# Optimization experiments

Hardware: AMD Instinct MI355X
Metric: run time of the kernel (lower is better)

## Reference

```python
import jax, jax.numpy as jnp
from jax import lax
import numpy as np

IN, HID, OUT = 28, 64, 10


def _lstm_layer(x_seq, W_ih, W_hh, b_ih, b_hh):
    # x_seq: [B, T, in]; PyTorch gate order: i, f, g, o (stacked along 4H)
    B = x_seq.shape[0]
    H = W_hh.shape[1]
    # Precompute input projection for all timesteps: [B, T, 4H]
    x_proj = jnp.einsum('bti,gi->btg', x_seq, W_ih) + b_ih + b_hh

    def step(carry, xt):
        h, c = carry
        gates = xt + h @ W_hh.T  # [B, 4H]
        i, f, g, o = jnp.split(gates, 4, axis=-1)
        i = jax.nn.sigmoid(i)
        f = jax.nn.sigmoid(f)
        g = jnp.tanh(g)
        o = jax.nn.sigmoid(o)
        c = f * c + i * g
        h = o * jnp.tanh(c)
        return (h, c), h

    h0 = jnp.zeros((B, H), x_seq.dtype)
    (_, _), hs = lax.scan(step, (h0, h0), jnp.swapaxes(x_proj, 0, 1))
    return jnp.swapaxes(hs, 0, 1)  # [B, T, H]


def setup_inputs() -> dict:
    key = jax.random.key(0)
    ks = jax.random.split(key, 12)
    s_in = 1.0 / np.sqrt(HID)
    u = lambda k, shape: jax.random.uniform(k, shape, jnp.float32, -s_in, s_in)
    return {
        'x': jax.random.normal(ks[0], (16384, 1, 28, 28), jnp.float32),
        'W_ih0': u(ks[1], (4 * HID, IN)),
        'W_hh0': u(ks[2], (4 * HID, HID)),
        'b_ih0': u(ks[3], (4 * HID,)),
        'b_hh0': u(ks[4], (4 * HID,)),
        'W_ih1': u(ks[5], (4 * HID, HID)),
        'W_hh1': u(ks[6], (4 * HID, HID)),
        'b_ih1': u(ks[7], (4 * HID,)),
        'b_hh1': u(ks[8], (4 * HID,)),
        'W_lin': u(ks[9], (OUT, HID)),
        'b_lin': u(ks[10], (OUT,)),
    }


def reference(x, W_ih0, W_hh0, b_ih0, b_hh0, W_ih1, W_hh1, b_ih1, b_hh1, W_lin, b_lin):
    # (N, C, H, W) -> (N, C*H, W): sequence of rows, feature = W = 28
    x = x.reshape(x.shape[0], -1, x.shape[-1])
    h1 = _lstm_layer(x, W_ih0, W_hh0, b_ih0, b_hh0)   # [B, T, 64]
    h2 = _lstm_layer(h1, W_ih1, W_hh1, b_ih1, b_hh1)  # [B, T, 64]
    last = h2[:, -1, :]
    return last @ W_lin.T + b_lin  # [B, 10]
```

## Files before the change

kernel.cpp:

```cpp
#include <hip/hip_runtime.h>


typedef _Float16 half8 __attribute__((ext_vector_type(8)));
typedef float floatx4 __attribute__((ext_vector_type(4)));

__device__ __forceinline__ float sigf(float v) {
    return __builtin_amdgcn_rcpf(1.0f + __expf(-v));
}
__device__ __forceinline__ float tanhf2(float v) {
    return 1.0f - 2.0f * __builtin_amdgcn_rcpf(__expf(2.0f * v) + 1.0f);
}

__launch_bounds__(512, 4)
__global__ void lstm_mfma(const float* __restrict__ x,
                          const float* __restrict__ Wih0, const float* __restrict__ Whh0,
                          const float* __restrict__ bih0, const float* __restrict__ bhh0,
                          const float* __restrict__ Wih1, const float* __restrict__ Whh1,
                          const float* __restrict__ bih1, const float* __restrict__ bhh1,
                          const float* __restrict__ Wlin, const float* __restrict__ blin,
                          float* __restrict__ out) {
    __shared__ __align__(16) _Float16 h0p[2][2048];
    __shared__ __align__(16) _Float16 h1p[2][2048];
    __shared__ __align__(16) _Float16 xb[2][1024];
    __shared__ float wlin_s[640];
    __shared__ float blin_s[10];

    const int lane = threadIdx.x;
    const int w    = threadIdx.y;
    const int tid  = w * 64 + lane;
    const int quad = lane >> 4;
    const int col  = lane & 15;

    half8 A0[2][3], A1[2][4];
    #pragma unroll
    for (int im = 0; im < 2; ++im) {
        int mt = 2 * w + im;
        int m  = mt * 16 + col;
        int u  = m >> 2, g = m & 3;
        int row = g * 64 + u;
        #pragma unroll
        for (int kt = 0; kt < 3; ++kt) {
            half8 r;
            #pragma unroll
            for (int j = 0; j < 8; ++j) {
                int k = kt * 32 + quad * 8 + j;
                float v;
                if (k < 28)       v = Wih0[row * 28 + k];
                else if (k == 28) v = bih0[row] + bhh0[row];
                else if (k < 32)  v = 0.f;
                else              v = Whh0[row * 64 + (k - 32)];
                r[j] = (_Float16)v;
            }
            A0[im][kt] = r;
        }
        #pragma unroll
        for (int kt = 0; kt < 4; ++kt) {
            half8 r;
            #pragma unroll
            for (int j = 0; j < 8; ++j) {
                int k = kt * 32 + quad * 8 + j;
                float v = (k < 64) ? Wih1[row * 64 + k] : Whh1[row * 64 + (k - 64)];
                r[j] = (_Float16)v;
            }
            A1[im][kt] = r;
        }
    }
    floatx4 bias1[2];
    #pragma unroll
    for (int im = 0; im < 2; ++im) {
        int u = (2 * w + im) * 4 + quad;
        #pragma unroll
        for (int r = 0; r < 4; ++r) bias1[im][r] = bih1[r * 64 + u] + bhh1[r * 64 + u];
    }

    int xrd[2], hrd[2][2], hwr[2][2];
    #pragma unroll
    for (int in = 0; in < 2; ++in) {
        xrd[in] = in * 512 + lane * 8;
        #pragma unroll
        for (int kt = 0; kt < 2; ++kt) hrd[kt][in] = (in * 2 + kt) * 512 + lane * 8;
        #pragma unroll
        for (int im = 0; im < 2; ++im) {
            int u = (2 * w + im) * 4 + quad;
            hwr[im][in] = (in * 2 + (u >> 5)) * 512 + (((u >> 3) & 3) * 16 + col) * 8 + (u & 7);
        }
    }

    const int xi = tid & 31;
    const bool xvalid = xi < 28;
    const float* xg[2];
    int xstg[2];
    #pragma unroll
    for (int s = 0; s < 2; ++s) {
        int b = (tid >> 5) + s * 16;
        xg[s]   = x + (blockIdx.x * 32 + b) * 784 + xi;
        xstg[s] = (b >> 4) * 512 + ((xi >> 3) * 16 + (b & 15)) * 8 + (xi & 7);
    }

    {
        int* z0 = (int*)&h0p[1][0];
        int* z1 = (int*)&h1p[1][0];
        #pragma unroll
        for (int i = tid; i < 1024; i += 512) { z0[i] = 0; z1[i] = 0; }
        #pragma unroll
        for (int s = 0; s < 2; ++s) {
            float xv = xvalid ? xg[s][0] : 0.f;
            xb[0][xstg[s]] = (xi == 28) ? (_Float16)1.0f : (_Float16)xv;
        }
    }
    __syncthreads();

    float c0[4] = {0.f, 0.f, 0.f, 0.f};
    float c1[4] = {0.f, 0.f, 0.f, 0.f};

    for (int p = -1; p <= 27; ++p) {
        const int pr  = p & 1;
        const int pr1 = pr ^ 1;
        const bool doL0 = (p < 27);
        const bool doL1 = (p >= 0);

        float xn[2] = {0.f, 0.f};
        if (p <= 25) {
            #pragma unroll
            for (int s = 0; s < 2; ++s)
                if (xvalid) xn[s] = xg[s][(p + 2) * 28];
        }

        half8 bh0[2][2];
        #pragma unroll
        for (int kt = 0; kt < 2; ++kt)
            #pragma unroll
            for (int in = 0; in < 2; ++in)
                bh0[kt][in] = *(const half8*)&h0p[pr][hrd[kt][in]];

        if (doL0) {
            floatx4 acc0[2][2];
            #pragma unroll
            for (int im = 0; im < 2; ++im)
                #pragma unroll
                for (int in = 0; in < 2; ++in)
                    acc0[im][in] = (floatx4){0.f, 0.f, 0.f, 0.f};
            #pragma unroll
            for (int in = 0; in < 2; ++in) {
                half8 bf = *(const half8*)&xb[pr1][xrd[in]];
                #pragma unroll
                for (int im = 0; im < 2; ++im)
                    acc0[im][in] = __builtin_amdgcn_mfma_f32_16x16x32_f16(A0[im][0], bf, acc0[im][in], 0, 0, 0);
            }
            #pragma unroll
            for (int kt = 0; kt < 2; ++kt)
                #pragma unroll
                for (int in = 0; in < 2; ++in)
                    #pragma unroll
                    for (int im = 0; im < 2; ++im)
                        acc0[im][in] = __builtin_amdgcn_mfma_f32_16x16x32_f16(A0[im][kt + 1], bh0[kt][in], acc0[im][in], 0, 0, 0);
            #pragma unroll
            for (int im = 0; im < 2; ++im) {
                #pragma unroll
                for (int in = 0; in < 2; ++in) {
                    floatx4 a = acc0[im][in];
                    float ig = sigf(a[0]), fg = sigf(a[1]), gg = tanhf2(a[2]), og = sigf(a[3]);
                    float c = fg * c0[im * 2 + in] + ig * gg;
                    c0[im * 2 + in] = c;
                    h0p[pr1][hwr[im][in]] = (_Float16)(og * tanhf2(c));
                }
            }
        }

        if (doL1) {
            floatx4 acc1[2][2];
            #pragma unroll
            for (int im = 0; im < 2; ++im)
                #pragma unroll
                for (int in = 0; in < 2; ++in)
                    acc1[im][in] = bias1[im];
            #pragma unroll
            for (int kt = 0; kt < 2; ++kt)
                #pragma unroll
                for (int in = 0; in < 2; ++in)
                    #pragma unroll
                    for (int im = 0; im < 2; ++im)
                        acc1[im][in] = __builtin_amdgcn_mfma_f32_16x16x32_f16(A1[im][kt], bh0[kt][in], acc1[im][in], 0, 0, 0);
            #pragma unroll
            for (int kt = 0; kt < 2; ++kt) {
                #pragma unroll
                for (int in = 0; in < 2; ++in) {
                    half8 bf = *(const half8*)&h1p[pr1][hrd[kt][in]];
                    #pragma unroll
                    for (int im = 0; im < 2; ++im)
                        acc1[im][in] = __builtin_amdgcn_mfma_f32_16x16x32_f16(A1[im][kt + 2], bf, acc1[im][in], 0, 0, 0);
                }
            }
            #pragma unroll
            for (int im = 0; im < 2; ++im) {
                #pragma unroll
                for (int in = 0; in < 2; ++in) {
                    floatx4 a = acc1[im][in];
                    float ig = sigf(a[0]), fg = sigf(a[1]), gg = tanhf2(a[2]), og = sigf(a[3]);
                    float c = fg * c1[im * 2 + in] + ig * gg;
                    c1[im * 2 + in] = c;
                    h1p[pr][hwr[im][in]] = (_Float16)(og * tanhf2(c));
                }
            }
        }

        if (p <= 25) {
            #pragma unroll
            for (int s = 0; s < 2; ++s)
                xb[pr][xstg[s]] = (xi == 28) ? (_Float16)1.0f : (_Float16)xn[s];
        }
        __syncthreads();
    }

    #pragma unroll
    for (int i = tid; i < 640; i += 512) wlin_s[i] = Wlin[i];
    if (tid < 10) blin_s[tid] = blin[tid];
    __syncthreads();
    if (tid < 320) {
        int b = tid / 10, o = tid - b * 10;
        float a = blin_s[o];
        #pragma unroll 8
        for (int u = 0; u < 64; ++u) {
            float hv = (float)h1p[1][((b >> 4) * 2 + (u >> 5)) * 512 + (((u >> 3) & 3) * 16 + (b & 15)) * 8 + (u & 7)];
            a += wlin_s[o * 64 + u] * hv;
        }
        out[(blockIdx.x * 32 + b) * 10 + o] = a;
    }
}

extern "C" void kernel_launch(void* const* d_in, const int* in_sizes, int n_in,
                              void* d_out, int out_size, void* d_ws, size_t ws_size,
                              hipStream_t stream) {
    const float* x    = (const float*)d_in[0];
    const float* Wih0 = (const float*)d_in[1];
    const float* Whh0 = (const float*)d_in[2];
    const float* bih0 = (const float*)d_in[3];
    const float* bhh0 = (const float*)d_in[4];
    const float* Wih1 = (const float*)d_in[5];
    const float* Whh1 = (const float*)d_in[6];
    const float* bih1 = (const float*)d_in[7];
    const float* bhh1 = (const float*)d_in[8];
    const float* Wlin = (const float*)d_in[9];
    const float* blin = (const float*)d_in[10];
    float* out = (float*)d_out;

    lstm_mfma<<<512, dim3(64, 8), 0, stream>>>(x, Wih0, Whh0, bih0, bhh0,
                                               Wih1, Whh1, bih1, bhh1, Wlin, blin, out);
}
```

Measured before the change: 197.9 us.

## Peel wavefront prologue/epilogue, interleave layer MFMAs, batch gate transcendentals

The skewed two-layer time loop is split into a peeled prologue (layer 0 only), a steady-state loop with no per-iteration branches, and a peeled epilogue (layer 1 only). In the steady state all LDS operands are loaded up front and the layer-0 and layer-1 MFMAs are interleaved so independent accumulator chains can overlap. Gate math is batched so all exps and reciprocals for the four tiles are issued together, raising instruction-level parallelism. Launch bounds drop from 4 to 2 blocks per CU, which allows more registers per thread but may lower occupancy.

```diff
diff --git a/kernel.cpp b/kernel.cpp
--- a/kernel.cpp
+++ b/kernel.cpp
@@ -4,14 +4,42 @@
 typedef _Float16 half8 __attribute__((ext_vector_type(8)));
 typedef float floatx4 __attribute__((ext_vector_type(4)));
 
-__device__ __forceinline__ float sigf(float v) {
-    return __builtin_amdgcn_rcpf(1.0f + __expf(-v));
+__device__ __forceinline__ void gate_batch4(const floatx4 (&acc)[2][2], float (&c)[4],
+                                            _Float16* __restrict__ plane,
+                                            const int (&hwr)[2][2]) {
+    float ei[4], ef[4], eg[4], eo[4];
+    #pragma unroll
+    for (int tt = 0; tt < 4; ++tt) {
+        floatx4 a = acc[tt >> 1][tt & 1];
+        ei[tt] = __expf(-a[0]);
+        ef[tt] = __expf(-a[1]);
+        eg[tt] = __expf(2.0f * a[2]);
+        eo[tt] = __expf(-a[3]);
+    }
+    float ri[4], rf[4], rg[4], ro[4];
+    #pragma unroll
+    for (int tt = 0; tt < 4; ++tt) {
+        ri[tt] = __builtin_amdgcn_rcpf(1.0f + ei[tt]);
+        rf[tt] = __builtin_amdgcn_rcpf(1.0f + ef[tt]);
+        rg[tt] = __builtin_amdgcn_rcpf(1.0f + eg[tt]);
+        ro[tt] = __builtin_amdgcn_rcpf(1.0f + eo[tt]);
+    }
+    float ec[4];
+    #pragma unroll
+    for (int tt = 0; tt < 4; ++tt) {
+        float tg = 1.0f - 2.0f * rg[tt];
+        float cn = rf[tt] * c[tt] + ri[tt] * tg;
+        c[tt] = cn;
+        ec[tt] = __expf(2.0f * cn);
+    }
+    #pragma unroll
+    for (int tt = 0; tt < 4; ++tt) {
+        float tc = 1.0f - 2.0f * __builtin_amdgcn_rcpf(ec[tt] + 1.0f);
+        plane[hwr[tt >> 1][tt & 1]] = (_Float16)(ro[tt] * tc);
+    }
 }
-__device__ __forceinline__ float tanhf2(float v) {
-    return 1.0f - 2.0f * __builtin_amdgcn_rcpf(__expf(2.0f * v) + 1.0f);
-}
-
-__launch_bounds__(512, 4)
+
+__launch_bounds__(512, 2)
 __global__ void lstm_mfma(const float* __restrict__ x,
                           const float* __restrict__ Wih0, const float* __restrict__ Whh0,
                           const float* __restrict__ bih0, const float* __restrict__ bhh0,
@@ -113,102 +141,122 @@
     float c0[4] = {0.f, 0.f, 0.f, 0.f};
     float c1[4] = {0.f, 0.f, 0.f, 0.f};
 
-    for (int p = -1; p <= 27; ++p) {
+    {
+        float xn[2] = {0.f, 0.f};
+        #pragma unroll
+        for (int s = 0; s < 2; ++s)
+            if (xvalid) xn[s] = xg[s][28];
+
+        floatx4 acc0[2][2];
+        #pragma unroll
+        for (int im = 0; im < 2; ++im)
+            #pragma unroll
+            for (int in = 0; in < 2; ++in)
+                acc0[im][in] = (floatx4){0.f, 0.f, 0.f, 0.f};
+        #pragma unroll
+        for (int in = 0; in < 2; ++in) {
+            half8 bf = *(const half8*)&xb[0][xrd[in]];
+            #pragma unroll
+            for (int im = 0; im < 2; ++im)
+                acc0[im][in] = __builtin_amdgcn_mfma_f32_16x16x32_f16(A0[im][0], bf, acc0[im][in], 0, 0, 0);
+        }
+        #pragma unroll
+        for (int kt = 0; kt < 2; ++kt) {
+            #pragma unroll
+            for (int in = 0; in < 2; ++in) {
+                half8 bf = *(const half8*)&h0p[1][hrd[kt][in]];
+                #pragma unroll
+                for (int im = 0; im < 2; ++im)
+                    acc0[im][in] = __builtin_amdgcn_mfma_f32_16x16x32_f16(A0[im][kt + 1], bf, acc0[im][in], 0, 0, 0);
+            }
+        }
+        gate_batch4(acc0, c0, &h0p[0][0], hwr);
+        #pragma unroll
+        for (int s = 0; s < 2; ++s)
+            xb[1][xstg[s]] = (xi == 28) ? (_Float16)1.0f : (_Float16)xn[s];
+        __syncthreads();
+    }
+
+    for (int p = 0; p < 27; ++p) {
         const int pr  = p & 1;
         const int pr1 = pr ^ 1;
-        const bool doL0 = (p < 27);
-        const bool doL1 = (p >= 0);
-
+        const _Float16* h0r = &h0p[pr][0];
+        _Float16*       h0w = &h0p[pr1][0];
+        const _Float16* h1r = &h1p[pr1][0];
+        _Float16*       h1w = &h1p[pr][0];
+        const _Float16* xr  = &xb[pr1][0];
+        _Float16*       xw  = &xb[pr][0];
+
+        const int xoff = (p < 26 ? p + 2 : 27) * 28;
         float xn[2] = {0.f, 0.f};
-        if (p <= 25) {
-            #pragma unroll
-            for (int s = 0; s < 2; ++s)
-                if (xvalid) xn[s] = xg[s][(p + 2) * 28];
-        }
-
-        half8 bh0[2][2];
+        #pragma unroll
+        for (int s = 0; s < 2; ++s)
+            if (xvalid) xn[s] = xg[s][xoff];
+
+        half8 bh0[2][2], bh1[2][2], bx[2];
+        #pragma unroll
+        for (int in = 0; in < 2; ++in) {
+            bx[in] = *(const half8*)&xr[xrd[in]];
+            #pragma unroll
+            for (int kt = 0; kt < 2; ++kt) {
+                bh0[kt][in] = *(const half8*)&h0r[hrd[kt][in]];
+                bh1[kt][in] = *(const half8*)&h1r[hrd[kt][in]];
+            }
+        }
+
+        floatx4 acc0[2][2], acc1[2][2];
+        #pragma unroll
+        for (int im = 0; im < 2; ++im)
+            #pragma unroll
+            for (int in = 0; in < 2; ++in) {
+                acc0[im][in] = (floatx4){0.f, 0.f, 0.f, 0.f};
+                acc1[im][in] = bias1[im];
+            }
+        #pragma unroll
+        for (int in = 0; in < 2; ++in)
+            #pragma unroll
+            for (int im = 0; im < 2; ++im)
+                acc0[im][in] = __builtin_amdgcn_mfma_f32_16x16x32_f16(A0[im][0], bx[in], acc0[im][in], 0, 0, 0);
         #pragma unroll
         for (int kt = 0; kt < 2; ++kt)
             #pragma unroll
             for (int in = 0; in < 2; ++in)
-                bh0[kt][in] = *(const half8*)&h0p[pr][hrd[kt][in]];
-
-        if (doL0) {
-            floatx4 acc0[2][2];
-            #pragma unroll
-            for (int im = 0; im < 2; ++im)
                 #pragma unroll
-                for (int in = 0; in < 2; ++in)
-                    acc0[im][in] = (floatx4){0.f, 0.f, 0.f, 0.f};
+                for (int im = 0; im < 2; ++im) {
+                    acc0[im][in] = __builtin_amdgcn_mfma_f32_16x16x32_f16(A0[im][kt + 1], bh0[kt][in], acc0[im][in], 0, 0, 0);
+                    acc1[im][in] = __builtin_amdgcn_mfma_f32_16x16x32_f16(A1[im][kt],     bh0[kt][in], acc1[im][in], 0, 0, 0);
+                    acc1[im][in] = __builtin_amdgcn_mfma_f32_16x16x32_f16(A1[im][kt + 2], bh1[kt][in], acc1[im][in], 0, 0, 0);
+                }
+
+        gate_batch4(acc0, c0, h0w, hwr);
+        gate_batch4(acc1, c1, h1w, hwr);
+        #pragma unroll
+        for (int s = 0; s < 2; ++s)
+            xw[xstg[s]] = (xi == 28) ? (_Float16)1.0f : (_Float16)xn[s];
+        __syncthreads();
+    }
+
+    {
+        floatx4 acc1[2][2];
+        #pragma unroll
+        for (int im = 0; im < 2; ++im)
+            #pragma unroll
+            for (int in = 0; in < 2; ++in)
+                acc1[im][in] = bias1[im];
+        #pragma unroll
+        for (int kt = 0; kt < 2; ++kt) {
             #pragma unroll
             for (int in = 0; in < 2; ++in) {
-                half8 bf = *(const half8*)&xb[pr1][xrd[in]];
+                half8 b0 = *(const half8*)&h0p[1][hrd[kt][in]];
+                half8 b1 = *(const half8*)&h1p[0][hrd[kt][in]];
                 #pragma unroll
-                for (int im = 0; im < 2; ++im)
-                    acc0[im][in] = __builtin_amdgcn_mfma_f32_16x16x32_f16(A0[im][0], bf, acc0[im][in], 0, 0, 0);
-            }
-            #pragma unroll
-            for (int kt = 0; kt < 2; ++kt)
-                #pragma unroll
-                for (int in = 0; in < 2; ++in)
-                    #pragma unroll
-                    for (int im = 0; im < 2; ++im)
-                        acc0[im][in] = __builtin_amdgcn_mfma_f32_16x16x32_f16(A0[im][kt + 1], bh0[kt][in], acc0[im][in], 0, 0, 0);
-            #pragma unroll
-            for (int im = 0; im < 2; ++im) {
-                #pragma unroll
-                for (int in = 0; in < 2; ++in) {
-                    floatx4 a = acc0[im][in];
-                    float ig = sigf(a[0]), fg = sigf(a[1]), gg = tanhf2(a[2]), og = sigf(a[3]);
-                    float c = fg * c0[im * 2 + in] + ig * gg;
-                    c0[im * 2 + in] = c;
-                    h0p[pr1][hwr[im][in]] = (_Float16)(og * tanhf2(c));
+                for (int im = 0; im < 2; ++im) {
+                    acc1[im][in] = __builtin_amdgcn_mfma_f32_16x16x32_f16(A1[im][kt],     b0, acc1[im][in], 0, 0, 0);
+                    acc1[im][in] = __builtin_amdgcn_mfma_f32_16x16x32_f16(A1[im][kt + 2], b1, acc1[im][in], 0, 0, 0);
                 }
             }
         }
-
-        if (doL1) {
-            floatx4 acc1[2][2];
-            #pragma unroll
-            for (int im = 0; im < 2; ++im)
-                #pragma unroll
-                for (int in = 0; in < 2; ++in)
-                    acc1[im][in] = bias1[im];
-            #pragma unroll
-            for (int kt = 0; kt < 2; ++kt)
-                #pragma unroll
-                for (int in = 0; in < 2; ++in)
-                    #pragma unroll
-                    for (int im = 0; im < 2; ++im)
-                        acc1[im][in] = __builtin_amdgcn_mfma_f32_16x16x32_f16(A1[im][kt], bh0[kt][in], acc1[im][in], 0, 0, 0);
-            #pragma unroll
-            for (int kt = 0; kt < 2; ++kt) {
-                #pragma unroll
-                for (int in = 0; in < 2; ++in) {
-                    half8 bf = *(const half8*)&h1p[pr1][hrd[kt][in]];
-                    #pragma unroll
-                    for (int im = 0; im < 2; ++im)
-                        acc1[im][in] = __builtin_amdgcn_mfma_f32_16x16x32_f16(A1[im][kt + 2], bf, acc1[im][in], 0, 0, 0);
-                }
-            }
-            #pragma unroll
-            for (int im = 0; im < 2; ++im) {
-                #pragma unroll
-                for (int in = 0; in < 2; ++in) {
-                    floatx4 a = acc1[im][in];
-                    float ig = sigf(a[0]), fg = sigf(a[1]), gg = tanhf2(a[2]), og = sigf(a[3]);
-                    float c = fg * c1[im * 2 + in] + ig * gg;
-                    c1[im * 2 + in] = c;
-                    h1p[pr][hwr[im][in]] = (_Float16)(og * tanhf2(c));
-                }
-            }
-        }
-
-        if (p <= 25) {
-            #pragma unroll
-            for (int s = 0; s < 2; ++s)
-                xb[pr][xstg[s]] = (xi == 28) ? (_Float16)1.0f : (_Float16)xn[s];
-        }
+        gate_batch4(acc1, c1, &h1p[1][0], hwr);
         __syncthreads();
     }
 
```

New measurement: 209.2 us. +5.7%, slower.
